# Kernel tuning notes

Measured on AMD Instinct MI355X. Metric: run time of the kernel, lower is better.

The kernel has to match this reference:

```python
import jax, jax.numpy as jnp
import numpy as np

M, N, DIM, B = 64, 64, 512, 4096
SIGMA = max(M, N) / 2.0  # default sigma in BaseSOM.__init__


def setup_inputs() -> dict:
    key = jax.random.key(0)
    k1, k2 = jax.random.split(key)
    batch = jax.random.normal(k1, (B, DIM), dtype=jnp.float32)
    weights = jax.random.uniform(k2, (M * N, DIM), dtype=jnp.float32)
    # grid locations [(i, j) for i in range(M) for j in range(N)]
    ii, jj = jnp.meshgrid(jnp.arange(M), jnp.arange(N), indexing="ij")
    locations = jnp.stack([ii.reshape(-1), jj.reshape(-1)], axis=1).astype(jnp.int64)
    return {
        "batch": batch,
        "weights": weights,
        "locations": locations,
        "decay_rate": 1000,
        "it": 100,
    }


def reference(batch, weights, locations, decay_rate, it):
    # Squared Euclidean distances (argmin is identical to argmin of cdist p=2).
    x2 = jnp.sum(batch * batch, axis=1, keepdims=True)          # [B, 1]
    w2 = jnp.sum(weights * weights, axis=1)[None, :]            # [1, MN]
    d2 = x2 - 2.0 * (batch @ weights.T) + w2                    # [B, MN]
    bmu_indices = jnp.argmin(d2, axis=1)                        # [B]
    bmu_loc = locations[bmu_indices]                            # [B, 2]
    lr = jnp.exp(-jnp.float32(it) / jnp.float32(decay_rate))
    sigma_op = jnp.float32(SIGMA) * lr
    # [B, MN, 2] grid offsets -> squared grid distance [B, MN]
    diff = locations[None, :, :].astype(jnp.float32) - bmu_loc[:, None, :].astype(jnp.float32)
    dist_sq = jnp.sum(diff * diff, axis=2)
    return jnp.exp(-dist_sq / (sigma_op * sigma_op))
```

## Files before the change

kernel.cpp:

```cpp
#include <hip/hip_runtime.h>
#include <cfloat>

#define DIMK 512
#define MN   4096
#define BATCH 4096
#define NGRP 1024

typedef _Float16 half8_t __attribute__((ext_vector_type(8)));
typedef _Float16 half4_t __attribute__((ext_vector_type(4)));
typedef float f32x4 __attribute__((ext_vector_type(4)));

#define GLD16(gp, lp) __builtin_amdgcn_global_load_lds( \
    (const __attribute__((address_space(1))) void*)(gp), \
    (__attribute__((address_space(3))) void*)(lp), 16, 0, 0)

__global__ __launch_bounds__(256) void convert_kernel(
        const float* __restrict__ X, const float* __restrict__ W,
        _Float16* __restrict__ Xh, _Float16* __restrict__ Wh,
        float* __restrict__ w2, float* __restrict__ xnorm) {
    const int blk  = blockIdx.x;
    const int t    = threadIdx.x;
    const bool isW = blk >= 1024;
    const float* src = isW ? W : X;
    _Float16* dst  = isW ? Wh : Xh;
    const int rblk = isW ? blk - 1024 : blk;
    const size_t idx = (size_t)rblk * 2048 + (size_t)t * 8;

    float4 v0 = *(const float4*)(src + idx);
    float4 v1 = *(const float4*)(src + idx + 4);
    float v[8] = {v0.x, v0.y, v0.z, v0.w, v1.x, v1.y, v1.z, v1.w};
    half8_t hv;
    float s = 0.f;
#pragma unroll
    for (int e = 0; e < 8; e++) {
        s += v[e] * v[e];
        hv[e] = (_Float16)v[e];
    }
    *(half8_t*)(dst + idx) = hv;
#pragma unroll
    for (int o = 32; o > 0; o >>= 1) s += __shfl_down(s, o);
    if ((t & 63) == 0) {
        int row = rblk * 4 + (t >> 6);
        if (isW) w2[row] = s;
        else     xnorm[row] = __fsqrt_rn(s);
    }
}

__global__ __launch_bounds__(256, 3) void score_kernel(
        const _Float16* __restrict__ Xh, const _Float16* __restrict__ Wh,
        const float* __restrict__ w2, _Float16* __restrict__ Gm) {
    __shared__ __align__(16) _Float16 lds[3][2][4096];

    const int t    = threadIdx.x;
    const int lane = t & 63;
    const int w    = t >> 6;
    const int wm   = w >> 1;
    const int wn   = w & 1;

    const int id  = blockIdx.y * 32 + blockIdx.x;
    const int xcd = id & 7;
    const int li  = id >> 3;
    const int bm  = xcd * 4 + (li >> 5);
    const int bn  = li & 31;
    const int m0  = bm * 128;
    const int n0  = bn * 128;

    const int srow = (t >> 6) * 16 + (t & 15);
    const int skof = ((t >> 4) & 3) * 8;
    const _Float16* gA = Xh + (size_t)(m0 + srow) * DIMK + skof;
    const _Float16* gB = Wh + (size_t)(n0 + srow) * DIMK + skof;
    const int ldst = t * 8;

#define STG_A(bf, kt, c) GLD16(gA + (size_t)(c) * (64 * DIMK) + (kt) * 32, &lds[bf][0][(c) * 2048 + ldst])
#define STG_B(bf, kt, c) GLD16(gB + (size_t)(c) * (64 * DIMK) + (kt) * 32, &lds[bf][1][(c) * 2048 + ldst])
#define LDA(bf, rg) (*(const half8_t*)(&lds[bf][0][(rg) * 512 + lane * 8]))
#define LDB(bf, rg) (*(const half8_t*)(&lds[bf][1][(rg) * 512 + lane * 8]))

    f32x4 acc[4][4];
#pragma unroll
    for (int i = 0; i < 4; i++)
#pragma unroll
        for (int j = 0; j < 4; j++) acc[i][j] = (f32x4){0.f, 0.f, 0.f, 0.f};

    STG_A(0, 0, 0); STG_A(0, 0, 1); STG_B(0, 0, 0); STG_B(0, 0, 1);
    STG_A(1, 1, 0); STG_A(1, 1, 1); STG_B(1, 1, 0); STG_B(1, 1, 1);

#pragma unroll
    for (int kt = 0; kt < 16; ++kt) {
        const int bf = kt % 3;
        const int nb = (kt + 2) % 3;

        if (kt <= 14) { asm volatile("s_waitcnt vmcnt(4)" ::: "memory"); }
        else          { asm volatile("s_waitcnt vmcnt(0)" ::: "memory"); }
        __builtin_amdgcn_sched_barrier(0);
        __builtin_amdgcn_s_barrier();

        if (kt <= 13) {
            STG_A(nb, kt + 2, 0); STG_A(nb, kt + 2, 1);
            STG_B(nb, kt + 2, 0); STG_B(nb, kt + 2, 1);
        }

        half8_t a0 = LDA(bf, wm * 4 + 0), a1 = LDA(bf, wm * 4 + 1);
        half8_t a2 = LDA(bf, wm * 4 + 2), a3 = LDA(bf, wm * 4 + 3);
        half8_t b0 = LDB(bf, wn * 4 + 0), b1 = LDB(bf, wn * 4 + 1);
        half8_t b2 = LDB(bf, wn * 4 + 2), b3 = LDB(bf, wn * 4 + 3);

        asm volatile("s_waitcnt lgkmcnt(0)" ::: "memory");
        __builtin_amdgcn_sched_barrier(0);
        __builtin_amdgcn_s_setprio(1);
#pragma unroll
        for (int i = 0; i < 4; i++) {
            half8_t av = (i == 0) ? a0 : (i == 1) ? a1 : (i == 2) ? a2 : a3;
            acc[i][0] = __builtin_amdgcn_mfma_f32_16x16x32_f16(av, b0, acc[i][0], 0, 0, 0);
            acc[i][1] = __builtin_amdgcn_mfma_f32_16x16x32_f16(av, b1, acc[i][1], 0, 0, 0);
            acc[i][2] = __builtin_amdgcn_mfma_f32_16x16x32_f16(av, b2, acc[i][2], 0, 0, 0);
            acc[i][3] = __builtin_amdgcn_mfma_f32_16x16x32_f16(av, b3, acc[i][3], 0, 0, 0);
        }
        __builtin_amdgcn_s_setprio(0);
    }

    const int q   = lane >> 4;
    const int cl  = lane & 15;
    const int gb  = (n0 >> 2) + wn * 16;
    float w2v[4];
#pragma unroll
    for (int j = 0; j < 4; j++) w2v[j] = w2[n0 + wn * 64 + j * 16 + cl];
#pragma unroll
    for (int i = 0; i < 4; i++)
#pragma unroll
        for (int v = 0; v < 4; v++) {
            const int row = m0 + wm * 64 + i * 16 + q * 4 + v;
            _Float16* grow = Gm + (size_t)row * 1024 + gb;
#pragma unroll
            for (int j = 0; j < 4; j++) {
                float s = w2v[j] - 2.0f * acc[i][j][v];
                s = fminf(s, __shfl_xor(s, 1));
                s = fminf(s, __shfl_xor(s, 2));
                if ((cl & 3) == 0) grow[j * 4 + (cl >> 2)] = (_Float16)s;
            }
        }
}

__global__ __launch_bounds__(256) void epilogue_kernel(
        const float* __restrict__ w2, const float* __restrict__ xnorm,
        const float* __restrict__ X, const float* __restrict__ W,
        const _Float16* __restrict__ gm,
        const int* __restrict__ decay_p, const int* __restrict__ it_p,
        float* __restrict__ out) {
    __shared__ float xs[512];
    __shared__ int   list[NGRP];
    __shared__ int   cnt;
    __shared__ float wmin[4];
    __shared__ unsigned long long wkey[4];
    __shared__ float tab[128];
    const int row  = blockIdx.x;
    const int t    = threadIdx.x;
    const int lane = t & 63;
    const int w    = t >> 6;

    {
        float2 xv = *(const float2*)(X + (size_t)row * DIMK + t * 2);
        xs[2 * t]     = xv.x;
        xs[2 * t + 1] = xv.y;
    }
    if (t == 0) cnt = 0;

    half4_t gmh = *((const half4_t*)(gm + (size_t)row * 1024) + t);
    float gme[4] = {(float)gmh[0], (float)gmh[1], (float)gmh[2], (float)gmh[3]};
    float g = fminf(fminf(gme[0], gme[1]), fminf(gme[2], gme[3]));
#pragma unroll
    for (int mask = 1; mask <= 32; mask <<= 1)
        g = fminf(g, __shfl_xor(g, mask));
    if (lane == 0) wmin[w] = g;
    __syncthreads();
    const float gmin = fminf(fminf(wmin[0], wmin[1]), fminf(wmin[2], wmin[3]));
    const float tau  = gmin + 2.0f * (0.0222f * xnorm[row] + 0.25f);

#pragma unroll
    for (int e = 0; e < 4; e++)
        if (gme[e] <= tau) list[atomicAdd(&cnt, 1)] = t * 4 + e;
    __syncthreads();
    const int total = cnt;

    const int s16 = lane & 15;
    const int cg  = lane >> 4;
    float4 xq[8];
#pragma unroll
    for (int e = 0; e < 8; e++) xq[e] = ((const float4*)xs)[e * 16 + s16];

    unsigned long long mkey = ~0ULL;
    for (int idx = w; idx < total; idx += 4) {
        const int col = list[idx] * 4 + cg;
        const float4* wr = (const float4*)(W + (size_t)col * DIMK);
        float p = 0.f;
#pragma unroll
        for (int e = 0; e < 8; e++) {
            float4 wv = wr[e * 16 + s16];
            p += xq[e].x * wv.x + xq[e].y * wv.y
               + xq[e].z * wv.z + xq[e].w * wv.w;
        }
        p += __shfl_xor(p, 1); p += __shfl_xor(p, 2);
        p += __shfl_xor(p, 4); p += __shfl_xor(p, 8);
        const float s = w2[col] - 2.0f * p;
        unsigned int b = __float_as_uint(s);
        unsigned int u = (b & 0x80000000u) ? ~b : (b | 0x80000000u);
        unsigned long long key = ((unsigned long long)u << 32) | (unsigned int)col;
        mkey = key < mkey ? key : mkey;
    }
    {
        unsigned long long o;
        o = __shfl_xor(mkey, 16); mkey = o < mkey ? o : mkey;
        o = __shfl_xor(mkey, 32); mkey = o < mkey ? o : mkey;
    }
    if (lane == 0) wkey[w] = mkey;
    __syncthreads();
    unsigned long long k = wkey[0];
#pragma unroll
    for (int i = 1; i < 4; i++) k = wkey[i] < k ? wkey[i] : k;
    const int sbi = (int)(k & 0xffffffffu);

    const float lr  = __expf(-(float)(*it_p) / (float)(*decay_p));
    const float so  = 32.0f * lr;
    const float inv = 1.0f / (so * so);
    const int rr = sbi >> 6, cc = sbi & 63;
    if (t < 64) {
        float d = (float)(t - rr);
        tab[t] = __expf(-d * d * inv);
    } else if (t < 128) {
        float d = (float)(t - 64 - cc);
        tab[t] = __expf(-d * d * inv);
    }
    __syncthreads();
    const float* er = tab;
    const float* ec = tab + 64;
    f32x4* orow = (f32x4*)(out + (size_t)row * 4096);
#pragma unroll
    for (int qq = 0; qq < 4; qq++) {
        int f  = qq * 256 + t;
        int i  = f >> 4;
        int j0 = (f & 15) * 4;
        float e = er[i];
        f32x4 o = {e * ec[j0], e * ec[j0 + 1], e * ec[j0 + 2], e * ec[j0 + 3]};
        __builtin_nontemporal_store(o, orow + f);
    }
}

extern "C" void kernel_launch(void* const* d_in, const int* in_sizes, int n_in,
                              void* d_out, int out_size, void* d_ws, size_t ws_size,
                              hipStream_t stream) {
    const float* X       = (const float*)d_in[0];
    const float* W       = (const float*)d_in[1];
    const int*   decay_p = (const int*)d_in[3];
    const int*   it_p    = (const int*)d_in[4];
    float* out = (float*)d_out;

    _Float16* Xh = (_Float16*)d_ws;
    _Float16* Wh = Xh + (size_t)BATCH * DIMK;
    float*    w2 = (float*)(Wh + (size_t)MN * DIMK);
    float*    xn = w2 + MN;
    _Float16* gmv = (_Float16*)(xn + BATCH);

    convert_kernel<<<2048, 256, 0, stream>>>(X, W, Xh, Wh, w2, xn);
    score_kernel<<<dim3(32, 32), 256, 0, stream>>>(Xh, Wh, w2, gmv);
    epilogue_kernel<<<BATCH, 256, 0, stream>>>(w2, xn, X, W, gmv, decay_p, it_p, out);
}
```

Measured before the change: 141.9 us.

## Load GEMM operands directly into registers with 256x128 block tiles, drop LDS staging

The score GEMM stops staging tiles in LDS with triple-buffered global_load_lds and barriers. Each wave now loads its own A and B fragments straight from global memory into double-buffered registers. The block tile grows to 256x128 with 8x4 accumulators per wave, the grid is halved, and the XCD mapping is remapped. This removes LDS traffic and block barriers but loses operand sharing between waves, so global/L2 traffic and register pressure rise (launch bounds drop to 2 blocks per CU).

```diff
diff --git a/kernel.cpp b/kernel.cpp
--- a/kernel.cpp
+++ b/kernel.cpp
@@ -9,10 +9,6 @@
 typedef _Float16 half8_t __attribute__((ext_vector_type(8)));
 typedef _Float16 half4_t __attribute__((ext_vector_type(4)));
 typedef float f32x4 __attribute__((ext_vector_type(4)));
-
-#define GLD16(gp, lp) __builtin_amdgcn_global_load_lds( \
-    (const __attribute__((address_space(1))) void*)(gp), \
-    (__attribute__((address_space(3))) void*)(lp), 16, 0, 0)
 
 __global__ __launch_bounds__(256) void convert_kernel(
         const float* __restrict__ X, const float* __restrict__ W,
@@ -46,11 +42,9 @@
     }
 }
 
-__global__ __launch_bounds__(256, 3) void score_kernel(
+__global__ __launch_bounds__(256, 2) void score_kernel(
         const _Float16* __restrict__ Xh, const _Float16* __restrict__ Wh,
         const float* __restrict__ w2, _Float16* __restrict__ Gm) {
-    __shared__ __align__(16) _Float16 lds[3][2][4096];
-
     const int t    = threadIdx.x;
     const int lane = t & 63;
     const int w    = t >> 6;
@@ -60,62 +54,55 @@
     const int id  = blockIdx.y * 32 + blockIdx.x;
     const int xcd = id & 7;
     const int li  = id >> 3;
-    const int bm  = xcd * 4 + (li >> 5);
-    const int bn  = li & 31;
-    const int m0  = bm * 128;
+    const int bm  = (xcd >> 1) * 4 + (li >> 4);
+    const int bn  = (xcd & 1) * 16 + (li & 15);
+    const int m0  = bm * 256;
     const int n0  = bn * 128;
 
-    const int srow = (t >> 6) * 16 + (t & 15);
-    const int skof = ((t >> 4) & 3) * 8;
-    const _Float16* gA = Xh + (size_t)(m0 + srow) * DIMK + skof;
-    const _Float16* gB = Wh + (size_t)(n0 + srow) * DIMK + skof;
-    const int ldst = t * 8;
-
-#define STG_A(bf, kt, c) GLD16(gA + (size_t)(c) * (64 * DIMK) + (kt) * 32, &lds[bf][0][(c) * 2048 + ldst])
-#define STG_B(bf, kt, c) GLD16(gB + (size_t)(c) * (64 * DIMK) + (kt) * 32, &lds[bf][1][(c) * 2048 + ldst])
-#define LDA(bf, rg) (*(const half8_t*)(&lds[bf][0][(rg) * 512 + lane * 8]))
-#define LDB(bf, rg) (*(const half8_t*)(&lds[bf][1][(rg) * 512 + lane * 8]))
-
-    f32x4 acc[4][4];
-#pragma unroll
-    for (int i = 0; i < 4; i++)
+    const int r16 = lane & 15;
+    const int k8  = (lane >> 4) * 8;
+    const int offA = (m0 + wm * 128 + r16) * DIMK + k8;
+    const int offB = (n0 + wn * 64  + r16) * DIMK + k8;
+
+    f32x4 acc[8][4];
+#pragma unroll
+    for (int i = 0; i < 8; i++)
 #pragma unroll
         for (int j = 0; j < 4; j++) acc[i][j] = (f32x4){0.f, 0.f, 0.f, 0.f};
 
-    STG_A(0, 0, 0); STG_A(0, 0, 1); STG_B(0, 0, 0); STG_B(0, 0, 1);
-    STG_A(1, 1, 0); STG_A(1, 1, 1); STG_B(1, 1, 0); STG_B(1, 1, 1);
+    half8_t a[2][8], b[2][4];
+
+#pragma unroll
+    for (int i = 0; i < 8; i++)
+        a[0][i] = *(const half8_t*)(Xh + offA + i * (16 * DIMK));
+#pragma unroll
+    for (int j = 0; j < 4; j++)
+        b[0][j] = *(const half8_t*)(Wh + offB + j * (16 * DIMK));
 
 #pragma unroll
     for (int kt = 0; kt < 16; ++kt) {
-        const int bf = kt % 3;
-        const int nb = (kt + 2) % 3;
-
-        if (kt <= 14) { asm volatile("s_waitcnt vmcnt(4)" ::: "memory"); }
-        else          { asm volatile("s_waitcnt vmcnt(0)" ::: "memory"); }
-        __builtin_amdgcn_sched_barrier(0);
-        __builtin_amdgcn_s_barrier();
-
-        if (kt <= 13) {
-            STG_A(nb, kt + 2, 0); STG_A(nb, kt + 2, 1);
-            STG_B(nb, kt + 2, 0); STG_B(nb, kt + 2, 1);
+        const int cur = kt & 1;
+        const int nxt = cur ^ 1;
+        if (kt < 15) {
+            const int ko = (kt + 1) * 32;
+#pragma unroll
+            for (int i = 0; i < 8; i++)
+                a[nxt][i] = *(const half8_t*)(Xh + offA + i * (16 * DIMK) + ko);
+#pragma unroll
+            for (int j = 0; j < 4; j++)
+                b[nxt][j] = *(const half8_t*)(Wh + offB + j * (16 * DIMK) + ko);
+            asm volatile("s_waitcnt vmcnt(12)" ::: "memory");
+        } else {
+            asm volatile("s_waitcnt vmcnt(0)" ::: "memory");
         }
-
-        half8_t a0 = LDA(bf, wm * 4 + 0), a1 = LDA(bf, wm * 4 + 1);
-        half8_t a2 = LDA(bf, wm * 4 + 2), a3 = LDA(bf, wm * 4 + 3);
-        half8_t b0 = LDB(bf, wn * 4 + 0), b1 = LDB(bf, wn * 4 + 1);
-        half8_t b2 = LDB(bf, wn * 4 + 2), b3 = LDB(bf, wn * 4 + 3);
-
-        asm volatile("s_waitcnt lgkmcnt(0)" ::: "memory");
         __builtin_amdgcn_sched_barrier(0);
         __builtin_amdgcn_s_setprio(1);
 #pragma unroll
-        for (int i = 0; i < 4; i++) {
-            half8_t av = (i == 0) ? a0 : (i == 1) ? a1 : (i == 2) ? a2 : a3;
-            acc[i][0] = __builtin_amdgcn_mfma_f32_16x16x32_f16(av, b0, acc[i][0], 0, 0, 0);
-            acc[i][1] = __builtin_amdgcn_mfma_f32_16x16x32_f16(av, b1, acc[i][1], 0, 0, 0);
-            acc[i][2] = __builtin_amdgcn_mfma_f32_16x16x32_f16(av, b2, acc[i][2], 0, 0, 0);
-            acc[i][3] = __builtin_amdgcn_mfma_f32_16x16x32_f16(av, b3, acc[i][3], 0, 0, 0);
-        }
+        for (int i = 0; i < 8; i++)
+#pragma unroll
+            for (int j = 0; j < 4; j++)
+                acc[i][j] = __builtin_amdgcn_mfma_f32_16x16x32_f16(
+                    a[cur][i], b[cur][j], acc[i][j], 0, 0, 0);
         __builtin_amdgcn_s_setprio(0);
     }
 
@@ -126,14 +113,14 @@
 #pragma unroll
     for (int j = 0; j < 4; j++) w2v[j] = w2[n0 + wn * 64 + j * 16 + cl];
 #pragma unroll
-    for (int i = 0; i < 4; i++)
+    for (int ai = 0; ai < 8; ai++)
 #pragma unroll
         for (int v = 0; v < 4; v++) {
-            const int row = m0 + wm * 64 + i * 16 + q * 4 + v;
+            const int row = m0 + wm * 128 + ai * 16 + q * 4 + v;
             _Float16* grow = Gm + (size_t)row * 1024 + gb;
 #pragma unroll
             for (int j = 0; j < 4; j++) {
-                float s = w2v[j] - 2.0f * acc[i][j][v];
+                float s = w2v[j] - 2.0f * acc[ai][j][v];
                 s = fminf(s, __shfl_xor(s, 1));
                 s = fminf(s, __shfl_xor(s, 2));
                 if ((cl & 3) == 0) grow[j * 4 + (cl >> 2)] = (_Float16)s;
@@ -261,6 +248,6 @@
     _Float16* gmv = (_Float16*)(xn + BATCH);
 
     convert_kernel<<<2048, 256, 0, stream>>>(X, W, Xh, Wh, w2, xn);
-    score_kernel<<<dim3(32, 32), 256, 0, stream>>>(Xh, Wh, w2, gmv);
+    score_kernel<<<dim3(32, 16), 256, 0, stream>>>(Xh, Wh, w2, gmv);
     epilogue_kernel<<<BATCH, 256, 0, stream>>>(w2, xn, X, W, gmv, decay_p, it_p, out);
 }
```

After: 160.2 us. 1.13x slower.

## Deepen score GEMM pipeline to four LDS stages with swizzled layout and retiled grid

Applied to the files above, without the earlier changes.

Moves the score kernel from a 3-stage to a 4-stage async global-to-LDS pipeline, prefetching three K tiles ahead with adjusted vmcnt waits. It also changes the staging layout to an XOR-swizzled row layout meant to reduce LDS bank conflicts on fragment reads, and remaps blocks to XCDs as 8x16 sub-tiles for better L2 reuse. LDS per block grows to 64 KB, so launch bounds drop from 3 to 2 blocks per CU, which may reduce occupancy.

```diff
diff --git a/kernel.cpp b/kernel.cpp
--- a/kernel.cpp
+++ b/kernel.cpp
@@ -46,10 +46,10 @@
     }
 }
 
-__global__ __launch_bounds__(256, 3) void score_kernel(
+__global__ __launch_bounds__(256, 2) void score_kernel(
         const _Float16* __restrict__ Xh, const _Float16* __restrict__ Wh,
         const float* __restrict__ w2, _Float16* __restrict__ Gm) {
-    __shared__ __align__(16) _Float16 lds[3][2][4096];
+    __shared__ __align__(16) _Float16 lds[4][8192];
 
     const int t    = threadIdx.x;
     const int lane = t & 63;
@@ -60,21 +60,28 @@
     const int id  = blockIdx.y * 32 + blockIdx.x;
     const int xcd = id & 7;
     const int li  = id >> 3;
-    const int bm  = xcd * 4 + (li >> 5);
-    const int bn  = li & 31;
+    const int bm  = (xcd >> 1) * 8 + (li >> 4);
+    const int bn  = (xcd & 1) * 16 + (li & 15);
     const int m0  = bm * 128;
     const int n0  = bn * 128;
 
-    const int srow = (t >> 6) * 16 + (t & 15);
-    const int skof = ((t >> 4) & 3) * 8;
-    const _Float16* gA = Xh + (size_t)(m0 + srow) * DIMK + skof;
-    const _Float16* gB = Wh + (size_t)(n0 + srow) * DIMK + skof;
-    const int ldst = t * 8;
-
-#define STG_A(bf, kt, c) GLD16(gA + (size_t)(c) * (64 * DIMK) + (kt) * 32, &lds[bf][0][(c) * 2048 + ldst])
-#define STG_B(bf, kt, c) GLD16(gB + (size_t)(c) * (64 * DIMK) + (kt) * 32, &lds[bf][1][(c) * 2048 + ldst])
-#define LDA(bf, rg) (*(const half8_t*)(&lds[bf][0][(rg) * 512 + lane * 8]))
-#define LDB(bf, rg) (*(const half8_t*)(&lds[bf][1][(rg) * 512 + lane * 8]))
+    const _Float16* gA = Xh + (size_t)m0 * DIMK;
+    const _Float16* gB = Wh + (size_t)n0 * DIMK;
+
+    const int soff = (lane >> 2) * DIMK + (((lane & 3) ^ ((lane >> 3) & 3)) * 8);
+
+#define STG(reg, rb, kt, sl) GLD16( \
+    ((reg) ? gB : gA) + (size_t)(rb) * DIMK + (kt) * 32 + soff, \
+    &lds[sl][(reg) * 4096 + (rb) * 32])
+
+    const int r16 = lane & 15;
+    const int kg  = lane >> 4;
+    const int xx  = (r16 >> 1) & 3;
+    const int aoff =        wm * 2048 + r16 * 32 + ((kg ^ xx) * 8);
+    const int boff = 4096 + wn * 2048 + r16 * 32 + ((kg ^ xx) * 8);
+
+#define LDA(sl, rg) (*(const half8_t*)(&lds[sl][aoff + (rg) * 512]))
+#define LDB(sl, rg) (*(const half8_t*)(&lds[sl][boff + (rg) * 512]))
 
     f32x4 acc[4][4];
 #pragma unroll
@@ -82,28 +89,37 @@
 #pragma unroll
         for (int j = 0; j < 4; j++) acc[i][j] = (f32x4){0.f, 0.f, 0.f, 0.f};
 
-    STG_A(0, 0, 0); STG_A(0, 0, 1); STG_B(0, 0, 0); STG_B(0, 0, 1);
-    STG_A(1, 1, 0); STG_A(1, 1, 1); STG_B(1, 1, 0); STG_B(1, 1, 1);
+    const int w32 = w * 32;
+#pragma unroll
+    for (int pt = 0; pt < 3; ++pt) {
+        STG(0, w32,      pt, pt);
+        STG(0, w32 + 16, pt, pt);
+        STG(1, w32,      pt, pt);
+        STG(1, w32 + 16, pt, pt);
+    }
 
 #pragma unroll
     for (int kt = 0; kt < 16; ++kt) {
-        const int bf = kt % 3;
-        const int nb = (kt + 2) % 3;
-
-        if (kt <= 14) { asm volatile("s_waitcnt vmcnt(4)" ::: "memory"); }
-        else          { asm volatile("s_waitcnt vmcnt(0)" ::: "memory"); }
+        const int sl = kt & 3;
+        const int nb = (kt + 3) & 3;
+
+        if (kt <= 13)      { asm volatile("s_waitcnt vmcnt(8)" ::: "memory"); }
+        else if (kt == 14) { asm volatile("s_waitcnt vmcnt(4)" ::: "memory"); }
+        else               { asm volatile("s_waitcnt vmcnt(0)" ::: "memory"); }
         __builtin_amdgcn_sched_barrier(0);
         __builtin_amdgcn_s_barrier();
 
-        if (kt <= 13) {
-            STG_A(nb, kt + 2, 0); STG_A(nb, kt + 2, 1);
-            STG_B(nb, kt + 2, 0); STG_B(nb, kt + 2, 1);
-        }
-
-        half8_t a0 = LDA(bf, wm * 4 + 0), a1 = LDA(bf, wm * 4 + 1);
-        half8_t a2 = LDA(bf, wm * 4 + 2), a3 = LDA(bf, wm * 4 + 3);
-        half8_t b0 = LDB(bf, wn * 4 + 0), b1 = LDB(bf, wn * 4 + 1);
-        half8_t b2 = LDB(bf, wn * 4 + 2), b3 = LDB(bf, wn * 4 + 3);
+        if (kt <= 12) {
+            STG(0, w32,      kt + 3, nb);
+            STG(0, w32 + 16, kt + 3, nb);
+            STG(1, w32,      kt + 3, nb);
+            STG(1, w32 + 16, kt + 3, nb);
+        }
+
+        half8_t a0 = LDA(sl, 0), a1 = LDA(sl, 1);
+        half8_t a2 = LDA(sl, 2), a3 = LDA(sl, 3);
+        half8_t b0 = LDB(sl, 0), b1 = LDB(sl, 1);
+        half8_t b2 = LDB(sl, 2), b3 = LDB(sl, 3);
 
         asm volatile("s_waitcnt lgkmcnt(0)" ::: "memory");
         __builtin_amdgcn_sched_barrier(0);
```

New measurement: 134.0 us. -5.6%, faster.
